# Kernel tuning notes

Hardware: AMD Instinct MI355X
Metric: run time of the kernel (lower is better)

The kernel has to match this reference:

```python
import jax, jax.numpy as jnp
import numpy as np

N, E, IN_DIM, HID = 100000, 1000000, 128, 64


def setup_inputs() -> dict:
    key = jax.random.key(0)
    ks = jax.random.split(key, 9)
    x = jax.random.normal(ks[0], (N, IN_DIM), dtype=jnp.float32)
    edge_index = jax.random.randint(ks[1], (2, E), 0, N, dtype=jnp.int32)
    edge_weight = jax.random.uniform(ks[2], (E,), dtype=jnp.float32)
    # GCNConv / Linear parameters (glorot-ish scaling)
    W1 = jax.random.normal(ks[3], (IN_DIM, HID), dtype=jnp.float32) / np.sqrt(IN_DIM)
    b1 = jnp.zeros((HID,), jnp.float32)
    W2 = jax.random.normal(ks[4], (HID, HID), dtype=jnp.float32) / np.sqrt(HID)
    b2 = jnp.zeros((HID,), jnp.float32)
    Wl = jax.random.normal(ks[5], (HID, 1), dtype=jnp.float32) / np.sqrt(HID)
    bl = jnp.zeros((1,), jnp.float32)
    return {"x": x, "edge_index": edge_index, "edge_weight": edge_weight,
            "W1": W1, "b1": b1, "W2": W2, "b2": b2, "Wl": Wl, "bl": bl}


def _propagate(h, src, dst, norm, num_nodes):
    # gather neighbor features, weight by norm, scatter-add to destinations
    msg = h[src] * norm[:, None]  # [E+N, HID]
    return jax.ops.segment_sum(msg, dst, num_segments=num_nodes)


def reference(x, edge_index, edge_weight, W1, b1, W2, b2, Wl, bl):
    n = x.shape[0]
    loop = jnp.arange(n, dtype=edge_index.dtype)
    # add self-loops with weight 1 (PyG GCNConv default)
    src = jnp.concatenate([edge_index[0], loop])
    dst = jnp.concatenate([edge_index[1], loop])
    ew = jnp.concatenate([edge_weight, jnp.ones((n,), x.dtype)])
    # symmetric normalization: D^-1/2 A D^-1/2
    deg = jax.ops.segment_sum(ew, dst, num_segments=n)
    dinv = jnp.where(deg > 0, jax.lax.rsqrt(deg), 0.0)
    norm = dinv[src] * ew * dinv[dst]  # [E+N]

    h = _propagate(x @ W1, src, dst, norm, n) + b1
    h = jax.nn.relu(h)  # dropout is identity in eval mode
    h = _propagate(h @ W2, src, dst, norm, n) + b2
    h = jax.nn.relu(h)
    return (h @ Wl + bl).squeeze(-1)  # [N]
```

## Files before the change

kernel.cpp:

```cpp
#include <hip/hip_runtime.h>

#define IN_DIM 128
#define HID    64
#define SCAN_B 256
#define RSIZE  16384
#define CSHIFT 14
#define CSIZE  (1 << CSHIFT)
#define NCMAX  64

typedef __attribute__((ext_vector_type(4))) _Float16 f16x4;
typedef __attribute__((ext_vector_type(8))) _Float16 f16x8;
typedef __attribute__((ext_vector_type(4))) float    f32x4;

__global__ void k_prep_w(const float* __restrict__ W1, const float* __restrict__ W2,
                         _Float16* __restrict__ W1T, _Float16* __restrict__ W2T) {
    int i = blockIdx.x * blockDim.x + threadIdx.x;
    if (i < IN_DIM * HID) { int k = i >> 6, c = i & 63; W1T[c * IN_DIM + k] = (_Float16)W1[i]; }
    if (i < HID * HID)    { int k = i >> 6, c = i & 63; W2T[c * HID + k]    = (_Float16)W2[i]; }
}

__global__ __launch_bounds__(256) void k_bin_hist(const int* __restrict__ dst,
                                                  unsigned short* __restrict__ hist16,
                                                  int* __restrict__ rank,
                                                  int n, int e) {
    __shared__ int cnt[RSIZE];
    int c = blockIdx.x, r = blockIdx.y;
    int tid = threadIdx.x;
    int4* c4 = (int4*)cnt;
    #pragma unroll
    for (int k = 0; k < RSIZE / 4 / 256; ++k) c4[tid + k * 256] = make_int4(0, 0, 0, 0);
    __syncthreads();

    int base = r * RSIZE;
    int i0 = c << CSHIFT;
    int i1 = min(e, i0 + CSIZE);
    for (int i = i0 + tid; i < i1; i += 256) {
        int d = dst[i];
        unsigned rel = (unsigned)(d - base);
        if (rel < RSIZE) rank[i] = atomicAdd(&cnt[rel], 1);
    }
    __syncthreads();

    size_t hb = (size_t)c * n;
    for (int j = tid; j < RSIZE; j += 256) {
        int v = base + j;
        if (v < n) hist16[hb + v] = (unsigned short)cnt[j];
    }
}

__global__ void k_chunk_scan(unsigned short* __restrict__ hist16,
                             int* __restrict__ offsets, int n, int nc) {
    int v = blockIdx.x * blockDim.x + threadIdx.x;
    if (v >= n) return;
    int run = 0;
    for (int c = 0; c < nc; ++c) {
        size_t idx = (size_t)c * n + v;
        int t = hist16[idx];
        hist16[idx] = (unsigned short)run;
        run += t;
    }
    offsets[v] = run;
}

__global__ __launch_bounds__(SCAN_B) void k_scan1(int* __restrict__ data,
                                                  int* __restrict__ blockSums, int n) {
    __shared__ int s[SCAN_B];
    int tid = threadIdx.x;
    int gid = blockIdx.x * SCAN_B + tid;
    int v = (gid < n) ? data[gid] : 0;
    s[tid] = v;
    __syncthreads();
    for (int off = 1; off < SCAN_B; off <<= 1) {
        int t = (tid >= off) ? s[tid - off] : 0;
        __syncthreads();
        s[tid] += t;
        __syncthreads();
    }
    if (gid < n) data[gid] = s[tid] - v;
    if (tid == SCAN_B - 1) blockSums[blockIdx.x] = s[tid];
}

__global__ __launch_bounds__(512) void k_scan2(int* __restrict__ blockSums, int nb) {
    __shared__ int s[512];
    int tid = threadIdx.x;
    int v = (tid < nb) ? blockSums[tid] : 0;
    s[tid] = v;
    __syncthreads();
    for (int off = 1; off < 512; off <<= 1) {
        int t = (tid >= off) ? s[tid - off] : 0;
        __syncthreads();
        s[tid] += t;
        __syncthreads();
    }
    if (tid < nb) blockSums[tid] = s[tid] - v;
}

__global__ __launch_bounds__(SCAN_B) void k_scan3(int* __restrict__ data,
                                                  const int* __restrict__ blockSums,
                                                  int n, int e) {
    int gid = blockIdx.x * SCAN_B + threadIdx.x;
    if (gid < n) {
        data[gid] += blockSums[blockIdx.x];
        if (gid == n - 1) data[n] = e;
    }
}

__global__ void k_scatter(const int* __restrict__ src, const int* __restrict__ dst,
                          const float* __restrict__ ew, const int* __restrict__ rank,
                          const int* __restrict__ offsets,
                          const unsigned short* __restrict__ hist16,
                          int2* __restrict__ sedge, int n, int e) {
    int i = blockIdx.x * blockDim.x + threadIdx.x;
    if (i >= e) return;
    int d = dst[i];
    int c = i >> CSHIFT;
    int pos = offsets[d] + (int)hist16[(size_t)c * n + d] + rank[i];
    sedge[pos] = make_int2(src[i], __float_as_int(ew[i]));
}

__global__ void k_deg_dinv(const int* __restrict__ rowOff, const int2* __restrict__ sedge,
                           float* __restrict__ dinv, int n) {
    int v = blockIdx.x * blockDim.x + threadIdx.x;
    if (v >= n) return;
    int s = rowOff[v], t = rowOff[v + 1];
    float a = 1.0f;
    for (int j = s; j < t; ++j) a += __int_as_float(sedge[j].y);
    dinv[v] = rsqrtf(a);
}


__global__ __launch_bounds__(256) void k_gemm1(const float* __restrict__ x,
                                               const _Float16* __restrict__ W1T,
                                               const float* __restrict__ dinv,
                                               _Float16* __restrict__ h0, int n) {
    __shared__ _Float16 sX[4][16 * IN_DIM];
    int tid  = threadIdx.x;
    int wave = tid >> 6, lane = tid & 63;
    int row0 = blockIdx.x * 64 + wave * 16;
    int col  = lane & 15, kg = lane >> 4;

    f16x8 bfrag[4][4];
    #pragma unroll
    for (int ks = 0; ks < 4; ++ks)
        #pragma unroll
        for (int ct = 0; ct < 4; ++ct)
            bfrag[ks][ct] = *(const f16x8*)(W1T + (ct * 16 + col) * IN_DIM + ks * 32 + kg * 8);

    _Float16* myX = sX[wave];
    #pragma unroll
    for (int it = 0; it < 8; ++it) {
        int idx = it * 64 + lane;
        int r = idx >> 5, c4 = idx & 31;
        int grow = row0 + r;
        float4 v = make_float4(0.f, 0.f, 0.f, 0.f);
        if (grow < n) v = ((const float4*)x)[(size_t)grow * 32 + c4];
        f16x4 h; h.x = (_Float16)v.x; h.y = (_Float16)v.y; h.z = (_Float16)v.z; h.w = (_Float16)v.w;
        int off = (r * 256 + c4 * 8) ^ ((r & 7) << 4);
        *(f16x4*)((char*)myX + off) = h;
    }
    __syncthreads();

    f32x4 acc[4];
    #pragma unroll
    for (int ct = 0; ct < 4; ++ct) acc[ct] = (f32x4){0.f, 0.f, 0.f, 0.f};

    int arow = lane & 15;
    #pragma unroll
    for (int ks = 0; ks < 4; ++ks) {
        int off = (arow * 256 + kg * 16 + ks * 64) ^ ((arow & 7) << 4);
        f16x8 af = *(const f16x8*)((const char*)myX + off);
        #pragma unroll
        for (int ct = 0; ct < 4; ++ct)
            acc[ct] = __builtin_amdgcn_mfma_f32_16x16x32_f16(af, bfrag[ks][ct], acc[ct], 0, 0, 0);
    }

    int crow0 = row0 + kg * 4;
    #pragma unroll
    for (int r = 0; r < 4; ++r) {
        int gr = crow0 + r;
        if (gr < n) {
            float dv = dinv[gr];
            #pragma unroll
            for (int ct = 0; ct < 4; ++ct)
                h0[(size_t)gr * HID + ct * 16 + col] = (_Float16)(acc[ct][r] * dv);
        }
    }
}


__global__ __launch_bounds__(256) void k_gemm2(const _Float16* __restrict__ h1,
                                               const _Float16* __restrict__ W2T,
                                               const float* __restrict__ dinv,
                                               _Float16* __restrict__ h2, int n) {
    __shared__ _Float16 sX[4][16 * HID];
    int tid  = threadIdx.x;
    int wave = tid >> 6, lane = tid & 63;
    int row0 = blockIdx.x * 64 + wave * 16;
    int col  = lane & 15, kg = lane >> 4;

    f16x8 bfrag[2][4];
    #pragma unroll
    for (int ks = 0; ks < 2; ++ks)
        #pragma unroll
        for (int ct = 0; ct < 4; ++ct)
            bfrag[ks][ct] = *(const f16x8*)(W2T + (ct * 16 + col) * HID + ks * 32 + kg * 8);

    _Float16* myX = sX[wave];
    #pragma unroll
    for (int it = 0; it < 4; ++it) {
        int idx = it * 64 + lane;
        int r = idx >> 4, c4 = idx & 15;
        int grow = row0 + r;
        f16x4 h = (f16x4){0, 0, 0, 0};
        if (grow < n) h = ((const f16x4*)h1)[(size_t)grow * 16 + c4];
        int off = (r * 128 + c4 * 8) ^ ((r & 7) << 4);
        *(f16x4*)((char*)myX + off) = h;
    }
    __syncthreads();

    f32x4 acc[4];
    #pragma unroll
    for (int ct = 0; ct < 4; ++ct) acc[ct] = (f32x4){0.f, 0.f, 0.f, 0.f};

    int arow = lane & 15;
    #pragma unroll
    for (int ks = 0; ks < 2; ++ks) {
        int off = (arow * 128 + kg * 16 + ks * 64) ^ ((arow & 7) << 4);
        f16x8 af = *(const f16x8*)((const char*)myX + off);
        #pragma unroll
        for (int ct = 0; ct < 4; ++ct)
            acc[ct] = __builtin_amdgcn_mfma_f32_16x16x32_f16(af, bfrag[ks][ct], acc[ct], 0, 0, 0);
    }

    int crow0 = row0 + kg * 4;
    #pragma unroll
    for (int r = 0; r < 4; ++r) {
        int gr = crow0 + r;
        if (gr < n) {
            float dv = dinv[gr];
            #pragma unroll
            for (int ct = 0; ct < 4; ++ct)
                h2[(size_t)gr * HID + ct * 16 + col] = (_Float16)(acc[ct][r] * dv);
        }
    }
}


__global__ __launch_bounds__(256) void k_prop1(const int* __restrict__ rowOff,
                                               const int2* __restrict__ sedge,
                                               const _Float16* __restrict__ hin,
                                               const float* __restrict__ dinv,
                                               const float* __restrict__ b1,
                                               _Float16* __restrict__ hout, int n) {
    int wave = (blockIdx.x * blockDim.x + threadIdx.x) >> 6;
    int lane = threadIdx.x & 63;
    int g    = lane >> 3;
    int gl   = lane & 7;
    int node = wave * 8 + g;
    bool valid = node < n;
    int nd = valid ? node : 0;

    int start = rowOff[nd];
    int end   = valid ? rowOff[nd + 1] : start;
    float di  = dinv[nd];
    float4 bbA = ((const float4*)b1)[gl * 2];
    float4 bbB = ((const float4*)b1)[gl * 2 + 1];

    f16x8 sv = *(const f16x8*)(hin + (size_t)nd * HID + gl * 8);
    float a[8];
    #pragma unroll
    for (int t = 0; t < 8; ++t) a[t] = (float)sv[t];

    int j = start;
    for (; j + 4 <= end; j += 4) {
        int2 e0 = sedge[j], e1 = sedge[j + 1], e2 = sedge[j + 2], e3 = sedge[j + 3];
        f16x8 v0 = *(const f16x8*)(hin + (size_t)e0.x * HID + gl * 8);
        f16x8 v1 = *(const f16x8*)(hin + (size_t)e1.x * HID + gl * 8);
        f16x8 v2 = *(const f16x8*)(hin + (size_t)e2.x * HID + gl * 8);
        f16x8 v3 = *(const f16x8*)(hin + (size_t)e3.x * HID + gl * 8);
        float w0 = __int_as_float(e0.y), w1 = __int_as_float(e1.y);
        float w2 = __int_as_float(e2.y), w3 = __int_as_float(e3.y);
        #pragma unroll
        for (int t = 0; t < 8; ++t) a[t] = fmaf((float)v0[t], w0, a[t]);
        #pragma unroll
        for (int t = 0; t < 8; ++t) a[t] = fmaf((float)v1[t], w1, a[t]);
        #pragma unroll
        for (int t = 0; t < 8; ++t) a[t] = fmaf((float)v2[t], w2, a[t]);
        #pragma unroll
        for (int t = 0; t < 8; ++t) a[t] = fmaf((float)v3[t], w3, a[t]);
    }
    if (j < end) {
        #pragma unroll
        for (int k = 0; k < 4; ++k) {
            int idx = j + k;
            int cl  = idx < end ? idx : j;
            int2 ed = sedge[cl];
            float w = idx < end ? __int_as_float(ed.y) : 0.0f;
            f16x8 v = *(const f16x8*)(hin + (size_t)ed.x * HID + gl * 8);
            #pragma unroll
            for (int t = 0; t < 8; ++t) a[t] = fmaf((float)v[t], w, a[t]);
        }
    }

    if (valid) {
        f16x8 o;
        o[0] = (_Float16)fmaxf(fmaf(a[0], di, bbA.x), 0.0f);
        o[1] = (_Float16)fmaxf(fmaf(a[1], di, bbA.y), 0.0f);
        o[2] = (_Float16)fmaxf(fmaf(a[2], di, bbA.z), 0.0f);
        o[3] = (_Float16)fmaxf(fmaf(a[3], di, bbA.w), 0.0f);
        o[4] = (_Float16)fmaxf(fmaf(a[4], di, bbB.x), 0.0f);
        o[5] = (_Float16)fmaxf(fmaf(a[5], di, bbB.y), 0.0f);
        o[6] = (_Float16)fmaxf(fmaf(a[6], di, bbB.z), 0.0f);
        o[7] = (_Float16)fmaxf(fmaf(a[7], di, bbB.w), 0.0f);
        *(f16x8*)(hout + (size_t)node * HID + gl * 8) = o;
    }
}

__global__ __launch_bounds__(256) void k_prop2_final(const int* __restrict__ rowOff,
                                                     const int2* __restrict__ sedge,
                                                     const _Float16* __restrict__ hin,
                                                     const float* __restrict__ dinv,
                                                     const float* __restrict__ b2,
                                                     const float* __restrict__ Wl,
                                                     const float* __restrict__ bl,
                                                     float* __restrict__ out, int n) {
    int wave = (blockIdx.x * blockDim.x + threadIdx.x) >> 6;
    int lane = threadIdx.x & 63;
    int g    = lane >> 3;
    int gl   = lane & 7;
    int node = wave * 8 + g;
    bool valid = node < n;
    int nd = valid ? node : 0;

    int start = rowOff[nd];
    int end   = valid ? rowOff[nd + 1] : start;
    float di  = dinv[nd];
    float4 bbA = ((const float4*)b2)[gl * 2];
    float4 bbB = ((const float4*)b2)[gl * 2 + 1];
    float4 wlA = ((const float4*)Wl)[gl * 2];
    float4 wlB = ((const float4*)Wl)[gl * 2 + 1];

    f16x8 sv = *(const f16x8*)(hin + (size_t)nd * HID + gl * 8);
    float a[8];
    #pragma unroll
    for (int t = 0; t < 8; ++t) a[t] = (float)sv[t];

    int j = start;
    for (; j + 4 <= end; j += 4) {
        int2 e0 = sedge[j], e1 = sedge[j + 1], e2 = sedge[j + 2], e3 = sedge[j + 3];
        f16x8 v0 = *(const f16x8*)(hin + (size_t)e0.x * HID + gl * 8);
        f16x8 v1 = *(const f16x8*)(hin + (size_t)e1.x * HID + gl * 8);
        f16x8 v2 = *(const f16x8*)(hin + (size_t)e2.x * HID + gl * 8);
        f16x8 v3 = *(const f16x8*)(hin + (size_t)e3.x * HID + gl * 8);
        float w0 = __int_as_float(e0.y), w1 = __int_as_float(e1.y);
        float w2 = __int_as_float(e2.y), w3 = __int_as_float(e3.y);
        #pragma unroll
        for (int t = 0; t < 8; ++t) a[t] = fmaf((float)v0[t], w0, a[t]);
        #pragma unroll
        for (int t = 0; t < 8; ++t) a[t] = fmaf((float)v1[t], w1, a[t]);
        #pragma unroll
        for (int t = 0; t < 8; ++t) a[t] = fmaf((float)v2[t], w2, a[t]);
        #pragma unroll
        for (int t = 0; t < 8; ++t) a[t] = fmaf((float)v3[t], w3, a[t]);
    }
    if (j < end) {
        #pragma unroll
        for (int k = 0; k < 4; ++k) {
            int idx = j + k;
            int cl  = idx < end ? idx : j;
            int2 ed = sedge[cl];
            float w = idx < end ? __int_as_float(ed.y) : 0.0f;
            f16x8 v = *(const f16x8*)(hin + (size_t)ed.x * HID + gl * 8);
            #pragma unroll
            for (int t = 0; t < 8; ++t) a[t] = fmaf((float)v[t], w, a[t]);
        }
    }

    float bb[8] = {bbA.x, bbA.y, bbA.z, bbA.w, bbB.x, bbB.y, bbB.z, bbB.w};
    float wl[8] = {wlA.x, wlA.y, wlA.z, wlA.w, wlB.x, wlB.y, wlB.z, wlB.w};
    float v = 0.0f;
    #pragma unroll
    for (int t = 0; t < 8; ++t)
        v += fmaxf(fmaf(a[t], di, bb[t]), 0.0f) * wl[t];
    #pragma unroll
    for (int off = 1; off < 8; off <<= 1)
        v += __shfl_xor(v, off);
    if (valid && gl == 0) out[node] = v + bl[0];
}


static inline char* align16(char* p) {
    return (char*)(((uintptr_t)p + 15) & ~(uintptr_t)15);
}

extern "C" void kernel_launch(void* const* d_in, const int* in_sizes, int n_in,
                              void* d_out, int out_size, void* d_ws, size_t ws_size,
                              hipStream_t stream) {
    const float* x   = (const float*)d_in[0];
    const int*   ei  = (const int*)d_in[1];
    const float* ew  = (const float*)d_in[2];
    const float* W1  = (const float*)d_in[3];
    const float* b1  = (const float*)d_in[4];
    const float* W2  = (const float*)d_in[5];
    const float* b2  = (const float*)d_in[6];
    const float* Wl  = (const float*)d_in[7];
    const float* bl  = (const float*)d_in[8];

    const int n = in_sizes[0] / IN_DIM;
    const int e = in_sizes[2];
    const int* src = ei;
    const int* dst = ei + e;

    float* out = (float*)d_out;
    const int B256 = 256;
    const int nScanBlocks = (n + SCAN_B - 1) / SCAN_B;
    const int nc = (e + CSIZE - 1) >> CSHIFT;
    const int nr = (n + RSIZE - 1) / RSIZE;

    char* p = (char*)d_ws;
    int2*           sedge   = (int2*)p;            p += (size_t)e * 8;
    float*          dinv    = (float*)p;           p += (size_t)n * 4;
    int*            offsets = (int*)p;             p += ((size_t)n + 1) * 4;
    p = align16(p);
    int*            bsums   = (int*)p;             p += 512 * 4;
    int*            rank    = (int*)p;             p += (size_t)e * 4;
    p = align16(p);
    unsigned short* hist16  = (unsigned short*)p;  p += (size_t)NCMAX * n * 2;
    _Float16*       W1T     = (_Float16*)p;        p += IN_DIM * HID * 2;
    _Float16*       W2T     = (_Float16*)p;        p += HID * HID * 2;
    p = align16(p);
    _Float16*       A       = (_Float16*)p;        p += (size_t)n * HID * 2;
    _Float16*       B       = (_Float16*)p;        p += (size_t)n * HID * 2;

    k_prep_w<<<(IN_DIM * HID + B256 - 1) / B256, B256, 0, stream>>>(W1, W2, W1T, W2T);

    dim3 binGrid(nc, nr);
    k_bin_hist<<<binGrid, B256, 0, stream>>>(dst, hist16, rank, n, e);

    k_chunk_scan<<<(n + B256 - 1) / B256, B256, 0, stream>>>(hist16, offsets, n, nc);

    k_scan1<<<nScanBlocks, SCAN_B, 0, stream>>>(offsets, bsums, n);
    k_scan2<<<1, 512, 0, stream>>>(bsums, nScanBlocks);
    k_scan3<<<nScanBlocks, SCAN_B, 0, stream>>>(offsets, bsums, n, e);

    k_scatter<<<(e + B256 - 1) / B256, B256, 0, stream>>>(src, dst, ew, rank,
                                                         offsets, hist16, sedge, n, e);

    k_deg_dinv<<<(n + B256 - 1) / B256, B256, 0, stream>>>(offsets, sedge, dinv, n);

    const int gemmBlocks = (n + 63) / 64;
    const int propBlocks = (n + 31) / 32;

    k_gemm1<<<gemmBlocks, B256, 0, stream>>>(x, W1T, dinv, A, n);
    k_prop1<<<propBlocks, B256, 0, stream>>>(offsets, sedge, A, dinv, b1, B, n);

    k_gemm2<<<gemmBlocks, B256, 0, stream>>>(B, W2T, dinv, A, n);
    k_prop2_final<<<propBlocks, B256, 0, stream>>>(offsets, sedge, A, dinv,
                                                   b2, Wl, bl, out, n);
}
```

Measured before the change: 199.9 us.

## Fuse CSR build into cooperative kernel and unroll edge gather by eight

Merges weight prep, destination binning, chunk scan, the block-level scan, scatter and degree computation into one cooperative kernel separated by grid-wide syncs. This removes several dependent launches and the final scan pass by folding block sums into the offset lookups. The propagation kernels now gather eight neighbor rows per iteration instead of four, to keep more loads in flight. The cost is grid-sync overhead, fewer threads in the scatter phase, and extra register pressure in the propagation loops. A multi-kernel fallback is kept for when cooperative residency is not possible.

```diff
diff --git a/kernel.cpp b/kernel.cpp
--- a/kernel.cpp
+++ b/kernel.cpp
@@ -1,4 +1,7 @@
 #include <hip/hip_runtime.h>
+#include <hip/hip_cooperative_groups.h>
+
+namespace cg = cooperative_groups;
 
 #define IN_DIM 128
 #define HID    64
@@ -11,6 +14,119 @@
 typedef __attribute__((ext_vector_type(4))) _Float16 f16x4;
 typedef __attribute__((ext_vector_type(8))) _Float16 f16x8;
 typedef __attribute__((ext_vector_type(4))) float    f32x4;
+
+__global__ __launch_bounds__(256, 2) void k_build(
+    const float* __restrict__ W1, const float* __restrict__ W2,
+    _Float16* __restrict__ W1T, _Float16* __restrict__ W2T,
+    const int* __restrict__ src, const int* __restrict__ dst,
+    const float* __restrict__ ew,
+    unsigned short* __restrict__ hist16, int* __restrict__ rank,
+    int* __restrict__ offsets, int* __restrict__ bsums,
+    int2* __restrict__ sedge, float* __restrict__ dinv,
+    int n, int e, int nc, int nr, int nTiles)
+{
+    __shared__ int cnt[RSIZE];
+    cg::grid_group grid = cg::this_grid();
+    const int nb  = nc * nr;
+    const int b   = blockIdx.x;
+    const int tid = threadIdx.x;
+
+    if (b < nb) {
+        int c = b % nc, r = b / nc;
+        int4* c4 = (int4*)cnt;
+        #pragma unroll
+        for (int k = tid; k < RSIZE / 4; k += 256) c4[k] = make_int4(0, 0, 0, 0);
+        __syncthreads();
+        int base = r * RSIZE;
+        int i0 = c << CSHIFT;
+        int i1 = min(e, i0 + CSIZE);
+        for (int i = i0 + tid; i < i1; i += 256) {
+            int d = dst[i];
+            unsigned rel = (unsigned)(d - base);
+            if (rel < RSIZE) rank[i] = atomicAdd(&cnt[rel], 1);
+        }
+        __syncthreads();
+        size_t hb = (size_t)c * n;
+        for (int j = tid; j < RSIZE; j += 256) {
+            int v = base + j;
+            if (v < n) hist16[hb + v] = (unsigned short)cnt[j];
+        }
+    } else {
+        int t = (b - nb) * 256 + tid;
+        for (int i = t; i < IN_DIM * HID; i += 512) {
+            int k = i >> 6, c2 = i & 63;
+            W1T[c2 * IN_DIM + k] = (_Float16)W1[i];
+        }
+        for (int i = t; i < HID * HID; i += 512) {
+            int k = i >> 6, c2 = i & 63;
+            W2T[c2 * HID + k] = (_Float16)W2[i];
+        }
+    }
+    grid.sync();
+
+    int gt = b * 256 + tid;
+    int total = 0;
+    if (gt < n) {
+        int run = 0;
+        for (int c = 0; c < nc; ++c) {
+            size_t idx = (size_t)c * n + gt;
+            int t0 = hist16[idx];
+            hist16[idx] = (unsigned short)run;
+            run += t0;
+        }
+        total = run;
+    }
+    __syncthreads();
+    cnt[tid] = total;
+    __syncthreads();
+    for (int off = 1; off < 256; off <<= 1) {
+        int t2 = (tid >= off) ? cnt[tid - off] : 0;
+        __syncthreads();
+        cnt[tid] += t2;
+        __syncthreads();
+    }
+    if (gt < n) offsets[gt] = cnt[tid] - total;
+    if (tid == 255 && b < nTiles) bsums[b] = cnt[255];
+    grid.sync();
+
+    if (b == 0) {
+        int v0 = (2 * tid     < nTiles) ? bsums[2 * tid]     : 0;
+        int v1 = (2 * tid + 1 < nTiles) ? bsums[2 * tid + 1] : 0;
+        __syncthreads();
+        cnt[tid] = v0 + v1;
+        __syncthreads();
+        for (int off = 1; off < 256; off <<= 1) {
+            int t2 = (tid >= off) ? cnt[tid - off] : 0;
+            __syncthreads();
+            cnt[tid] += t2;
+            __syncthreads();
+        }
+        int pexcl = cnt[tid] - (v0 + v1);
+        if (2 * tid     < nTiles) bsums[2 * tid]     = pexcl;
+        if (2 * tid + 1 < nTiles) bsums[2 * tid + 1] = pexcl + v0;
+    }
+    grid.sync();
+
+    {
+        int stride = gridDim.x * 256;
+        for (int i = gt; i < e; i += stride) {
+            int d = dst[i];
+            int c = i >> CSHIFT;
+            int pos = offsets[d] + bsums[d >> 8] + (int)hist16[(size_t)c * n + d] + rank[i];
+            sedge[pos] = make_int2(src[i], __float_as_int(ew[i]));
+        }
+    }
+    grid.sync();
+
+    if (gt < n) {
+        int s0 = offsets[gt] + bsums[gt >> 8];
+        int s1 = (gt == n - 1) ? e : (offsets[gt + 1] + bsums[(gt + 1) >> 8]);
+        float a = 1.0f;
+        for (int j = s0; j < s1; ++j) a += __int_as_float(sedge[j].y);
+        dinv[gt] = rsqrtf(a);
+    }
+}
+
 
 __global__ void k_prep_w(const float* __restrict__ W1, const float* __restrict__ W2,
                          _Float16* __restrict__ W1T, _Float16* __restrict__ W2T) {
@@ -28,9 +144,8 @@
     int tid = threadIdx.x;
     int4* c4 = (int4*)cnt;
     #pragma unroll
-    for (int k = 0; k < RSIZE / 4 / 256; ++k) c4[tid + k * 256] = make_int4(0, 0, 0, 0);
-    __syncthreads();
-
+    for (int k = tid; k < RSIZE / 4; k += 256) c4[k] = make_int4(0, 0, 0, 0);
+    __syncthreads();
     int base = r * RSIZE;
     int i0 = c << CSHIFT;
     int i1 = min(e, i0 + CSIZE);
@@ -40,7 +155,6 @@
         if (rel < RSIZE) rank[i] = atomicAdd(&cnt[rel], 1);
     }
     __syncthreads();
-
     size_t hb = (size_t)c * n;
     for (int j = tid; j < RSIZE; j += 256) {
         int v = base + j;
@@ -95,36 +209,28 @@
     if (tid < nb) blockSums[tid] = s[tid] - v;
 }
 
-__global__ __launch_bounds__(SCAN_B) void k_scan3(int* __restrict__ data,
-                                                  const int* __restrict__ blockSums,
-                                                  int n, int e) {
-    int gid = blockIdx.x * SCAN_B + threadIdx.x;
-    if (gid < n) {
-        data[gid] += blockSums[blockIdx.x];
-        if (gid == n - 1) data[n] = e;
-    }
-}
-
-__global__ void k_scatter(const int* __restrict__ src, const int* __restrict__ dst,
-                          const float* __restrict__ ew, const int* __restrict__ rank,
-                          const int* __restrict__ offsets,
-                          const unsigned short* __restrict__ hist16,
-                          int2* __restrict__ sedge, int n, int e) {
+__global__ void k_scatter_fb(const int* __restrict__ src, const int* __restrict__ dst,
+                             const float* __restrict__ ew, const int* __restrict__ rank,
+                             const int* __restrict__ offsets, const int* __restrict__ bsums,
+                             const unsigned short* __restrict__ hist16,
+                             int2* __restrict__ sedge, int n, int e) {
     int i = blockIdx.x * blockDim.x + threadIdx.x;
     if (i >= e) return;
     int d = dst[i];
     int c = i >> CSHIFT;
-    int pos = offsets[d] + (int)hist16[(size_t)c * n + d] + rank[i];
+    int pos = offsets[d] + bsums[d >> 8] + (int)hist16[(size_t)c * n + d] + rank[i];
     sedge[pos] = make_int2(src[i], __float_as_int(ew[i]));
 }
 
-__global__ void k_deg_dinv(const int* __restrict__ rowOff, const int2* __restrict__ sedge,
-                           float* __restrict__ dinv, int n) {
+__global__ void k_deg_dinv_fb(const int* __restrict__ offsets, const int* __restrict__ bsums,
+                              const int2* __restrict__ sedge, float* __restrict__ dinv,
+                              int n, int e) {
     int v = blockIdx.x * blockDim.x + threadIdx.x;
     if (v >= n) return;
-    int s = rowOff[v], t = rowOff[v + 1];
+    int s0 = offsets[v] + bsums[v >> 8];
+    int s1 = (v == n - 1) ? e : (offsets[v + 1] + bsums[(v + 1) >> 8]);
     float a = 1.0f;
-    for (int j = s; j < t; ++j) a += __int_as_float(sedge[j].y);
+    for (int j = s0; j < s1; ++j) a += __int_as_float(sedge[j].y);
     dinv[v] = rsqrtf(a);
 }
 
@@ -187,7 +293,6 @@
     }
 }
 
-
 __global__ __launch_bounds__(256) void k_gemm2(const _Float16* __restrict__ h1,
                                                const _Float16* __restrict__ W2T,
                                                const float* __restrict__ dinv,
@@ -246,12 +351,13 @@
 }
 
 
-__global__ __launch_bounds__(256) void k_prop1(const int* __restrict__ rowOff,
+__global__ __launch_bounds__(256) void k_prop1(const int* __restrict__ offR,
+                                               const int* __restrict__ bsums,
                                                const int2* __restrict__ sedge,
                                                const _Float16* __restrict__ hin,
                                                const float* __restrict__ dinv,
                                                const float* __restrict__ b1,
-                                               _Float16* __restrict__ hout, int n) {
+                                               _Float16* __restrict__ hout, int n, int e) {
     int wave = (blockIdx.x * blockDim.x + threadIdx.x) >> 6;
     int lane = threadIdx.x & 63;
     int g    = lane >> 3;
@@ -260,9 +366,13 @@
     bool valid = node < n;
     int nd = valid ? node : 0;
 
-    int start = rowOff[nd];
-    int end   = valid ? rowOff[nd + 1] : start;
-    float di  = dinv[nd];
+    int start = offR[nd] + bsums[nd >> 8];
+    int end;
+    if (!valid)            end = start;
+    else if (nd == n - 1)  end = e;
+    else                   end = offR[nd + 1] + bsums[(nd + 1) >> 8];
+
+    float di = dinv[nd];
     float4 bbA = ((const float4*)b1)[gl * 2];
     float4 bbB = ((const float4*)b1)[gl * 2 + 1];
 
@@ -272,26 +382,22 @@
     for (int t = 0; t < 8; ++t) a[t] = (float)sv[t];
 
     int j = start;
-    for (; j + 4 <= end; j += 4) {
-        int2 e0 = sedge[j], e1 = sedge[j + 1], e2 = sedge[j + 2], e3 = sedge[j + 3];
-        f16x8 v0 = *(const f16x8*)(hin + (size_t)e0.x * HID + gl * 8);
-        f16x8 v1 = *(const f16x8*)(hin + (size_t)e1.x * HID + gl * 8);
-        f16x8 v2 = *(const f16x8*)(hin + (size_t)e2.x * HID + gl * 8);
-        f16x8 v3 = *(const f16x8*)(hin + (size_t)e3.x * HID + gl * 8);
-        float w0 = __int_as_float(e0.y), w1 = __int_as_float(e1.y);
-        float w2 = __int_as_float(e2.y), w3 = __int_as_float(e3.y);
-        #pragma unroll
-        for (int t = 0; t < 8; ++t) a[t] = fmaf((float)v0[t], w0, a[t]);
-        #pragma unroll
-        for (int t = 0; t < 8; ++t) a[t] = fmaf((float)v1[t], w1, a[t]);
-        #pragma unroll
-        for (int t = 0; t < 8; ++t) a[t] = fmaf((float)v2[t], w2, a[t]);
-        #pragma unroll
-        for (int t = 0; t < 8; ++t) a[t] = fmaf((float)v3[t], w3, a[t]);
+    for (; j + 8 <= end; j += 8) {
+        int2 ed[8]; f16x8 v[8]; float w[8];
+        #pragma unroll
+        for (int k = 0; k < 8; ++k) ed[k] = sedge[j + k];
+        #pragma unroll
+        for (int k = 0; k < 8; ++k) v[k] = *(const f16x8*)(hin + (size_t)ed[k].x * HID + gl * 8);
+        #pragma unroll
+        for (int k = 0; k < 8; ++k) w[k] = __int_as_float(ed[k].y);
+        #pragma unroll
+        for (int k = 0; k < 8; ++k)
+            #pragma unroll
+            for (int t = 0; t < 8; ++t) a[t] = fmaf((float)v[k][t], w[k], a[t]);
     }
     if (j < end) {
         #pragma unroll
-        for (int k = 0; k < 4; ++k) {
+        for (int k = 0; k < 8; ++k) {
             int idx = j + k;
             int cl  = idx < end ? idx : j;
             int2 ed = sedge[cl];
@@ -316,14 +422,15 @@
     }
 }
 
-__global__ __launch_bounds__(256) void k_prop2_final(const int* __restrict__ rowOff,
+__global__ __launch_bounds__(256) void k_prop2_final(const int* __restrict__ offR,
+                                                     const int* __restrict__ bsums,
                                                      const int2* __restrict__ sedge,
                                                      const _Float16* __restrict__ hin,
                                                      const float* __restrict__ dinv,
                                                      const float* __restrict__ b2,
                                                      const float* __restrict__ Wl,
                                                      const float* __restrict__ bl,
-                                                     float* __restrict__ out, int n) {
+                                                     float* __restrict__ out, int n, int e) {
     int wave = (blockIdx.x * blockDim.x + threadIdx.x) >> 6;
     int lane = threadIdx.x & 63;
     int g    = lane >> 3;
@@ -332,9 +439,13 @@
     bool valid = node < n;
     int nd = valid ? node : 0;
 
-    int start = rowOff[nd];
-    int end   = valid ? rowOff[nd + 1] : start;
-    float di  = dinv[nd];
+    int start = offR[nd] + bsums[nd >> 8];
+    int end;
+    if (!valid)            end = start;
+    else if (nd == n - 1)  end = e;
+    else                   end = offR[nd + 1] + bsums[(nd + 1) >> 8];
+
+    float di = dinv[nd];
     float4 bbA = ((const float4*)b2)[gl * 2];
     float4 bbB = ((const float4*)b2)[gl * 2 + 1];
     float4 wlA = ((const float4*)Wl)[gl * 2];
@@ -346,26 +457,22 @@
     for (int t = 0; t < 8; ++t) a[t] = (float)sv[t];
 
     int j = start;
-    for (; j + 4 <= end; j += 4) {
-        int2 e0 = sedge[j], e1 = sedge[j + 1], e2 = sedge[j + 2], e3 = sedge[j + 3];
-        f16x8 v0 = *(const f16x8*)(hin + (size_t)e0.x * HID + gl * 8);
-        f16x8 v1 = *(const f16x8*)(hin + (size_t)e1.x * HID + gl * 8);
-        f16x8 v2 = *(const f16x8*)(hin + (size_t)e2.x * HID + gl * 8);
-        f16x8 v3 = *(const f16x8*)(hin + (size_t)e3.x * HID + gl * 8);
-        float w0 = __int_as_float(e0.y), w1 = __int_as_float(e1.y);
-        float w2 = __int_as_float(e2.y), w3 = __int_as_float(e3.y);
-        #pragma unroll
-        for (int t = 0; t < 8; ++t) a[t] = fmaf((float)v0[t], w0, a[t]);
-        #pragma unroll
-        for (int t = 0; t < 8; ++t) a[t] = fmaf((float)v1[t], w1, a[t]);
-        #pragma unroll
-        for (int t = 0; t < 8; ++t) a[t] = fmaf((float)v2[t], w2, a[t]);
-        #pragma unroll
-        for (int t = 0; t < 8; ++t) a[t] = fmaf((float)v3[t], w3, a[t]);
+    for (; j + 8 <= end; j += 8) {
+        int2 ed[8]; f16x8 v[8]; float w[8];
+        #pragma unroll
+        for (int k = 0; k < 8; ++k) ed[k] = sedge[j + k];
+        #pragma unroll
+        for (int k = 0; k < 8; ++k) v[k] = *(const f16x8*)(hin + (size_t)ed[k].x * HID + gl * 8);
+        #pragma unroll
+        for (int k = 0; k < 8; ++k) w[k] = __int_as_float(ed[k].y);
+        #pragma unroll
+        for (int k = 0; k < 8; ++k)
+            #pragma unroll
+            for (int t = 0; t < 8; ++t) a[t] = fmaf((float)v[k][t], w[k], a[t]);
     }
     if (j < end) {
         #pragma unroll
-        for (int k = 0; k < 4; ++k) {
+        for (int k = 0; k < 8; ++k) {
             int idx = j + k;
             int cl  = idx < end ? idx : j;
             int2 ed = sedge[cl];
@@ -413,9 +520,10 @@
 
     float* out = (float*)d_out;
     const int B256 = 256;
-    const int nScanBlocks = (n + SCAN_B - 1) / SCAN_B;
     const int nc = (e + CSIZE - 1) >> CSHIFT;
     const int nr = (n + RSIZE - 1) / RSIZE;
+    const int nTiles = (n + 255) / 256;
+    const int buildBlocks = nc * nr + 2;
 
     char* p = (char*)d_ws;
     int2*           sedge   = (int2*)p;            p += (size_t)e * 8;
@@ -432,29 +540,43 @@
     _Float16*       A       = (_Float16*)p;        p += (size_t)n * HID * 2;
     _Float16*       B       = (_Float16*)p;        p += (size_t)n * HID * 2;
 
-    k_prep_w<<<(IN_DIM * HID + B256 - 1) / B256, B256, 0, stream>>>(W1, W2, W1T, W2T);
-
-    dim3 binGrid(nc, nr);
-    k_bin_hist<<<binGrid, B256, 0, stream>>>(dst, hist16, rank, n, e);
-
-    k_chunk_scan<<<(n + B256 - 1) / B256, B256, 0, stream>>>(hist16, offsets, n, nc);
-
-    k_scan1<<<nScanBlocks, SCAN_B, 0, stream>>>(offsets, bsums, n);
-    k_scan2<<<1, 512, 0, stream>>>(bsums, nScanBlocks);
-    k_scan3<<<nScanBlocks, SCAN_B, 0, stream>>>(offsets, bsums, n, e);
-
-    k_scatter<<<(e + B256 - 1) / B256, B256, 0, stream>>>(src, dst, ew, rank,
-                                                         offsets, hist16, sedge, n, e);
-
-    k_deg_dinv<<<(n + B256 - 1) / B256, B256, 0, stream>>>(offsets, sedge, dinv, n);
+    int dev = 0;
+    hipGetDevice(&dev);
+    int nCU = 0;
+    hipDeviceGetAttribute(&nCU, hipDeviceAttributeMultiprocessorCount, dev);
+    int maxB = 0;
+    hipOccupancyMaxActiveBlocksPerMultiprocessor(&maxB, k_build, 256, 0);
+    bool coop = (nCU > 0 && maxB * nCU >= buildBlocks) && nTiles <= 512;
+
+    if (coop) {
+        int n_ = n, e_ = e, nc_ = nc, nr_ = nr, nT_ = nTiles;
+        void* args[] = {(void*)&W1, (void*)&W2, (void*)&W1T, (void*)&W2T,
+                        (void*)&src, (void*)&dst, (void*)&ew,
+                        (void*)&hist16, (void*)&rank, (void*)&offsets, (void*)&bsums,
+                        (void*)&sedge, (void*)&dinv,
+                        (void*)&n_, (void*)&e_, (void*)&nc_, (void*)&nr_, (void*)&nT_};
+        hipLaunchCooperativeKernel(k_build, dim3(buildBlocks), dim3(256), args, 0, stream);
+    } else {
+        k_prep_w<<<(IN_DIM * HID + B256 - 1) / B256, B256, 0, stream>>>(W1, W2, W1T, W2T);
+        dim3 binGrid(nc, nr);
+        k_bin_hist<<<binGrid, B256, 0, stream>>>(dst, hist16, rank, n, e);
+        k_chunk_scan<<<(n + B256 - 1) / B256, B256, 0, stream>>>(hist16, offsets, n, nc);
+        k_scan1<<<nTiles, SCAN_B, 0, stream>>>(offsets, bsums, n);
+        k_scan2<<<1, 512, 0, stream>>>(bsums, nTiles);
+        k_scatter_fb<<<(e + B256 - 1) / B256, B256, 0, stream>>>(src, dst, ew, rank,
+                                                                offsets, bsums, hist16,
+                                                                sedge, n, e);
+        k_deg_dinv_fb<<<(n + B256 - 1) / B256, B256, 0, stream>>>(offsets, bsums,
+                                                                 sedge, dinv, n, e);
+    }
 
     const int gemmBlocks = (n + 63) / 64;
     const int propBlocks = (n + 31) / 32;
 
     k_gemm1<<<gemmBlocks, B256, 0, stream>>>(x, W1T, dinv, A, n);
-    k_prop1<<<propBlocks, B256, 0, stream>>>(offsets, sedge, A, dinv, b1, B, n);
+    k_prop1<<<propBlocks, B256, 0, stream>>>(offsets, bsums, sedge, A, dinv, b1, B, n, e);
 
     k_gemm2<<<gemmBlocks, B256, 0, stream>>>(B, W2T, dinv, A, n);
-    k_prop2_final<<<propBlocks, B256, 0, stream>>>(offsets, sedge, A, dinv,
-                                                   b2, Wl, bl, out, n);
-}
+    k_prop2_final<<<propBlocks, B256, 0, stream>>>(offsets, bsums, sedge, A, dinv,
+                                                   b2, Wl, bl, out, n, e);
+}
```

Result: slower. 434.8 us (+117.4%).

## Replace CSR build with two-level bucket sort and unroll propagation gather by 8

Applied to the files above, without the earlier changes.

Replaces the per-node histogram, multi-kernel scan and scatter CSR construction with a two-level bucket sort. Edges are first counted and scattered into coarse buckets of 256 destination nodes, then a per-bucket kernel does a fine local sort and also computes degrees and dinv. Weight transposition is folded into the count kernel, which cuts the launch count and the large hist16/rank traffic. The propagation loops now issue 8 gathers per iteration instead of 4 to raise memory-level parallelism, at the cost of more registers and nondeterministic edge order inside a node.

```diff
diff --git a/kernel.cpp b/kernel.cpp
--- a/kernel.cpp
+++ b/kernel.cpp
@@ -2,130 +2,137 @@
 
 #define IN_DIM 128
 #define HID    64
-#define SCAN_B 256
-#define RSIZE  16384
-#define CSHIFT 14
-#define CSIZE  (1 << CSHIFT)
-#define NCMAX  64
+#define NCHUNK 128
+#define BWSH   8
+#define BW     (1 << BWSH)
 
 typedef __attribute__((ext_vector_type(4))) _Float16 f16x4;
 typedef __attribute__((ext_vector_type(8))) _Float16 f16x8;
 typedef __attribute__((ext_vector_type(4))) float    f32x4;
 
-__global__ void k_prep_w(const float* __restrict__ W1, const float* __restrict__ W2,
-                         _Float16* __restrict__ W1T, _Float16* __restrict__ W2T) {
-    int i = blockIdx.x * blockDim.x + threadIdx.x;
-    if (i < IN_DIM * HID) { int k = i >> 6, c = i & 63; W1T[c * IN_DIM + k] = (_Float16)W1[i]; }
-    if (i < HID * HID)    { int k = i >> 6, c = i & 63; W2T[c * HID + k]    = (_Float16)W2[i]; }
-}
-
-__global__ __launch_bounds__(256) void k_bin_hist(const int* __restrict__ dst,
-                                                  unsigned short* __restrict__ hist16,
-                                                  int* __restrict__ rank,
-                                                  int n, int e) {
-    __shared__ int cnt[RSIZE];
-    int c = blockIdx.x, r = blockIdx.y;
-    int tid = threadIdx.x;
-    int4* c4 = (int4*)cnt;
-    #pragma unroll
-    for (int k = 0; k < RSIZE / 4 / 256; ++k) c4[tid + k * 256] = make_int4(0, 0, 0, 0);
-    __syncthreads();
-
-    int base = r * RSIZE;
-    int i0 = c << CSHIFT;
-    int i1 = min(e, i0 + CSIZE);
+__global__ __launch_bounds__(256) void k_bcount(const int* __restrict__ dst,
+                                                int* __restrict__ counts,
+                                                const float* __restrict__ W1,
+                                                const float* __restrict__ W2,
+                                                _Float16* __restrict__ W1T,
+                                                _Float16* __restrict__ W2T,
+                                                int e, int nbk, int ech) {
+    int c = blockIdx.x, tid = threadIdx.x;
+    if (c >= NCHUNK) {
+        int t = (c - NCHUNK) * 256 + tid;
+        for (int i = t; i < IN_DIM * HID; i += 512) {
+            int k = i >> 6, cc = i & 63;
+            W1T[cc * IN_DIM + k] = (_Float16)W1[i];
+        }
+        for (int i = t; i < HID * HID; i += 512) {
+            int k = i >> 6, cc = i & 63;
+            W2T[cc * HID + k] = (_Float16)W2[i];
+        }
+        return;
+    }
+    __shared__ int cnt[512];
+    cnt[tid] = 0; cnt[tid + 256] = 0;
+    __syncthreads();
+    int i0 = c * ech, i1 = min(e, i0 + ech);
+    for (int i = i0 + tid; i < i1; i += 256)
+        atomicAdd(&cnt[dst[i] >> BWSH], 1);
+    __syncthreads();
+    for (int b = tid; b < nbk; b += 256) counts[c * nbk + b] = cnt[b];
+}
+
+__global__ __launch_bounds__(512) void k_bscan(int* __restrict__ counts,
+                                               int* __restrict__ bstart,
+                                               int* __restrict__ offsets,
+                                               int n, int e, int nbk) {
+    __shared__ int s[512];
+    int b = threadIdx.x;
+    int run = 0;
+    if (b < nbk) {
+        for (int c = 0; c < NCHUNK; ++c) {
+            int t = counts[c * nbk + b];
+            counts[c * nbk + b] = run;
+            run += t;
+        }
+    }
+    s[b] = run;
+    __syncthreads();
+    for (int off = 1; off < 512; off <<= 1) {
+        int t = (b >= off) ? s[b - off] : 0;
+        __syncthreads();
+        s[b] += t;
+        __syncthreads();
+    }
+    int excl = s[b] - run;
+    if (b < nbk) {
+        bstart[b] = excl;
+        for (int c = 0; c < NCHUNK; ++c) counts[c * nbk + b] += excl;
+    }
+    if (b == 0) { bstart[nbk] = e; offsets[n] = e; }
+}
+
+__global__ __launch_bounds__(256) void k_bscatter(const int* __restrict__ src,
+                                                  const int* __restrict__ dst,
+                                                  const float* __restrict__ ew,
+                                                  const int* __restrict__ starts,
+                                                  int2* __restrict__ tmpe,
+                                                  unsigned short* __restrict__ tmpl,
+                                                  int e, int nbk, int ech) {
+    __shared__ int cur[512];
+    int c = blockIdx.x, tid = threadIdx.x;
+    for (int b = tid; b < nbk; b += 256) cur[b] = starts[c * nbk + b];
+    __syncthreads();
+    int i0 = c * ech, i1 = min(e, i0 + ech);
     for (int i = i0 + tid; i < i1; i += 256) {
         int d = dst[i];
-        unsigned rel = (unsigned)(d - base);
-        if (rel < RSIZE) rank[i] = atomicAdd(&cnt[rel], 1);
-    }
-    __syncthreads();
-
-    size_t hb = (size_t)c * n;
-    for (int j = tid; j < RSIZE; j += 256) {
-        int v = base + j;
-        if (v < n) hist16[hb + v] = (unsigned short)cnt[j];
-    }
-}
-
-__global__ void k_chunk_scan(unsigned short* __restrict__ hist16,
-                             int* __restrict__ offsets, int n, int nc) {
-    int v = blockIdx.x * blockDim.x + threadIdx.x;
-    if (v >= n) return;
-    int run = 0;
-    for (int c = 0; c < nc; ++c) {
-        size_t idx = (size_t)c * n + v;
-        int t = hist16[idx];
-        hist16[idx] = (unsigned short)run;
-        run += t;
-    }
-    offsets[v] = run;
-}
-
-__global__ __launch_bounds__(SCAN_B) void k_scan1(int* __restrict__ data,
-                                                  int* __restrict__ blockSums, int n) {
-    __shared__ int s[SCAN_B];
-    int tid = threadIdx.x;
-    int gid = blockIdx.x * SCAN_B + tid;
-    int v = (gid < n) ? data[gid] : 0;
-    s[tid] = v;
-    __syncthreads();
-    for (int off = 1; off < SCAN_B; off <<= 1) {
-        int t = (tid >= off) ? s[tid - off] : 0;
+        int b = d >> BWSH;
+        int pos = atomicAdd(&cur[b], 1);
+        tmpe[pos] = make_int2(src[i], __float_as_int(ew[i]));
+        tmpl[pos] = (unsigned short)(d & (BW - 1));
+    }
+}
+
+__global__ __launch_bounds__(256) void k_bfine(const int* __restrict__ bstart,
+                                               const int2* __restrict__ tmpe,
+                                               const unsigned short* __restrict__ tmpl,
+                                               int2* __restrict__ sedge,
+                                               int* __restrict__ offsets,
+                                               float* __restrict__ dinv, int n) {
+    __shared__ int   cnt[256];
+    __shared__ float wsum[256];
+    __shared__ int   lsc[256];
+    __shared__ int   cur[256];
+    int b = blockIdx.x, tid = threadIdx.x;
+    int bs = bstart[b], be = bstart[b + 1];
+    cnt[tid] = 0; wsum[tid] = 0.0f;
+    __syncthreads();
+    for (int j = bs + tid; j < be; j += 256) {
+        int ld = tmpl[j];
+        atomicAdd(&cnt[ld], 1);
+        atomicAdd(&wsum[ld], __int_as_float(tmpe[j].y));
+    }
+    __syncthreads();
+    int v = cnt[tid];
+    lsc[tid] = v;
+    __syncthreads();
+    for (int off = 1; off < 256; off <<= 1) {
+        int t = (tid >= off) ? lsc[tid - off] : 0;
         __syncthreads();
-        s[tid] += t;
+        lsc[tid] += t;
         __syncthreads();
     }
-    if (gid < n) data[gid] = s[tid] - v;
-    if (tid == SCAN_B - 1) blockSums[blockIdx.x] = s[tid];
-}
-
-__global__ __launch_bounds__(512) void k_scan2(int* __restrict__ blockSums, int nb) {
-    __shared__ int s[512];
-    int tid = threadIdx.x;
-    int v = (tid < nb) ? blockSums[tid] : 0;
-    s[tid] = v;
-    __syncthreads();
-    for (int off = 1; off < 512; off <<= 1) {
-        int t = (tid >= off) ? s[tid - off] : 0;
-        __syncthreads();
-        s[tid] += t;
-        __syncthreads();
-    }
-    if (tid < nb) blockSums[tid] = s[tid] - v;
-}
-
-__global__ __launch_bounds__(SCAN_B) void k_scan3(int* __restrict__ data,
-                                                  const int* __restrict__ blockSums,
-                                                  int n, int e) {
-    int gid = blockIdx.x * SCAN_B + threadIdx.x;
-    if (gid < n) {
-        data[gid] += blockSums[blockIdx.x];
-        if (gid == n - 1) data[n] = e;
-    }
-}
-
-__global__ void k_scatter(const int* __restrict__ src, const int* __restrict__ dst,
-                          const float* __restrict__ ew, const int* __restrict__ rank,
-                          const int* __restrict__ offsets,
-                          const unsigned short* __restrict__ hist16,
-                          int2* __restrict__ sedge, int n, int e) {
-    int i = blockIdx.x * blockDim.x + threadIdx.x;
-    if (i >= e) return;
-    int d = dst[i];
-    int c = i >> CSHIFT;
-    int pos = offsets[d] + (int)hist16[(size_t)c * n + d] + rank[i];
-    sedge[pos] = make_int2(src[i], __float_as_int(ew[i]));
-}
-
-__global__ void k_deg_dinv(const int* __restrict__ rowOff, const int2* __restrict__ sedge,
-                           float* __restrict__ dinv, int n) {
-    int v = blockIdx.x * blockDim.x + threadIdx.x;
-    if (v >= n) return;
-    int s = rowOff[v], t = rowOff[v + 1];
-    float a = 1.0f;
-    for (int j = s; j < t; ++j) a += __int_as_float(sedge[j].y);
-    dinv[v] = rsqrtf(a);
+    int excl = lsc[tid] - v;
+    int node = b * BW + tid;
+    if (node < n) {
+        offsets[node] = bs + excl;
+        dinv[node] = rsqrtf(1.0f + wsum[tid]);
+    }
+    cur[tid] = excl;
+    __syncthreads();
+    for (int j = bs + tid; j < be; j += 256) {
+        int ld = tmpl[j];
+        int pos = bs + atomicAdd(&cur[ld], 1);
+        sedge[pos] = tmpe[j];
+    }
 }
 
 
@@ -187,7 +194,6 @@
     }
 }
 
-
 __global__ __launch_bounds__(256) void k_gemm2(const _Float16* __restrict__ h1,
                                                const _Float16* __restrict__ W2T,
                                                const float* __restrict__ dinv,
@@ -246,7 +252,7 @@
 }
 
 
-__global__ __launch_bounds__(256) void k_prop1(const int* __restrict__ rowOff,
+__global__ __launch_bounds__(256) void k_prop1(const int* __restrict__ offR,
                                                const int2* __restrict__ sedge,
                                                const _Float16* __restrict__ hin,
                                                const float* __restrict__ dinv,
@@ -260,9 +266,10 @@
     bool valid = node < n;
     int nd = valid ? node : 0;
 
-    int start = rowOff[nd];
-    int end   = valid ? rowOff[nd + 1] : start;
-    float di  = dinv[nd];
+    int start = offR[nd];
+    int end   = valid ? offR[nd + 1] : start;
+
+    float di = dinv[nd];
     float4 bbA = ((const float4*)b1)[gl * 2];
     float4 bbB = ((const float4*)b1)[gl * 2 + 1];
 
@@ -272,26 +279,22 @@
     for (int t = 0; t < 8; ++t) a[t] = (float)sv[t];
 
     int j = start;
-    for (; j + 4 <= end; j += 4) {
-        int2 e0 = sedge[j], e1 = sedge[j + 1], e2 = sedge[j + 2], e3 = sedge[j + 3];
-        f16x8 v0 = *(const f16x8*)(hin + (size_t)e0.x * HID + gl * 8);
-        f16x8 v1 = *(const f16x8*)(hin + (size_t)e1.x * HID + gl * 8);
-        f16x8 v2 = *(const f16x8*)(hin + (size_t)e2.x * HID + gl * 8);
-        f16x8 v3 = *(const f16x8*)(hin + (size_t)e3.x * HID + gl * 8);
-        float w0 = __int_as_float(e0.y), w1 = __int_as_float(e1.y);
-        float w2 = __int_as_float(e2.y), w3 = __int_as_float(e3.y);
-        #pragma unroll
-        for (int t = 0; t < 8; ++t) a[t] = fmaf((float)v0[t], w0, a[t]);
-        #pragma unroll
-        for (int t = 0; t < 8; ++t) a[t] = fmaf((float)v1[t], w1, a[t]);
-        #pragma unroll
-        for (int t = 0; t < 8; ++t) a[t] = fmaf((float)v2[t], w2, a[t]);
-        #pragma unroll
-        for (int t = 0; t < 8; ++t) a[t] = fmaf((float)v3[t], w3, a[t]);
+    for (; j + 8 <= end; j += 8) {
+        int2 ed[8]; f16x8 v[8]; float w[8];
+        #pragma unroll
+        for (int k = 0; k < 8; ++k) ed[k] = sedge[j + k];
+        #pragma unroll
+        for (int k = 0; k < 8; ++k) v[k] = *(const f16x8*)(hin + (size_t)ed[k].x * HID + gl * 8);
+        #pragma unroll
+        for (int k = 0; k < 8; ++k) w[k] = __int_as_float(ed[k].y);
+        #pragma unroll
+        for (int k = 0; k < 8; ++k)
+            #pragma unroll
+            for (int t = 0; t < 8; ++t) a[t] = fmaf((float)v[k][t], w[k], a[t]);
     }
     if (j < end) {
         #pragma unroll
-        for (int k = 0; k < 4; ++k) {
+        for (int k = 0; k < 8; ++k) {
             int idx = j + k;
             int cl  = idx < end ? idx : j;
             int2 ed = sedge[cl];
@@ -316,7 +319,7 @@
     }
 }
 
-__global__ __launch_bounds__(256) void k_prop2_final(const int* __restrict__ rowOff,
+__global__ __launch_bounds__(256) void k_prop2_final(const int* __restrict__ offR,
                                                      const int2* __restrict__ sedge,
                                                      const _Float16* __restrict__ hin,
                                                      const float* __restrict__ dinv,
@@ -332,9 +335,10 @@
     bool valid = node < n;
     int nd = valid ? node : 0;
 
-    int start = rowOff[nd];
-    int end   = valid ? rowOff[nd + 1] : start;
-    float di  = dinv[nd];
+    int start = offR[nd];
+    int end   = valid ? offR[nd + 1] : start;
+
+    float di = dinv[nd];
     float4 bbA = ((const float4*)b2)[gl * 2];
     float4 bbB = ((const float4*)b2)[gl * 2 + 1];
     float4 wlA = ((const float4*)Wl)[gl * 2];
@@ -346,26 +350,22 @@
     for (int t = 0; t < 8; ++t) a[t] = (float)sv[t];
 
     int j = start;
-    for (; j + 4 <= end; j += 4) {
-        int2 e0 = sedge[j], e1 = sedge[j + 1], e2 = sedge[j + 2], e3 = sedge[j + 3];
-        f16x8 v0 = *(const f16x8*)(hin + (size_t)e0.x * HID + gl * 8);
-        f16x8 v1 = *(const f16x8*)(hin + (size_t)e1.x * HID + gl * 8);
-        f16x8 v2 = *(const f16x8*)(hin + (size_t)e2.x * HID + gl * 8);
-        f16x8 v3 = *(const f16x8*)(hin + (size_t)e3.x * HID + gl * 8);
-        float w0 = __int_as_float(e0.y), w1 = __int_as_float(e1.y);
-        float w2 = __int_as_float(e2.y), w3 = __int_as_float(e3.y);
-        #pragma unroll
-        for (int t = 0; t < 8; ++t) a[t] = fmaf((float)v0[t], w0, a[t]);
-        #pragma unroll
-        for (int t = 0; t < 8; ++t) a[t] = fmaf((float)v1[t], w1, a[t]);
-        #pragma unroll
-        for (int t = 0; t < 8; ++t) a[t] = fmaf((float)v2[t], w2, a[t]);
-        #pragma unroll
-        for (int t = 0; t < 8; ++t) a[t] = fmaf((float)v3[t], w3, a[t]);
+    for (; j + 8 <= end; j += 8) {
+        int2 ed[8]; f16x8 v[8]; float w[8];
+        #pragma unroll
+        for (int k = 0; k < 8; ++k) ed[k] = sedge[j + k];
+        #pragma unroll
+        for (int k = 0; k < 8; ++k) v[k] = *(const f16x8*)(hin + (size_t)ed[k].x * HID + gl * 8);
+        #pragma unroll
+        for (int k = 0; k < 8; ++k) w[k] = __int_as_float(ed[k].y);
+        #pragma unroll
+        for (int k = 0; k < 8; ++k)
+            #pragma unroll
+            for (int t = 0; t < 8; ++t) a[t] = fmaf((float)v[k][t], w[k], a[t]);
     }
     if (j < end) {
         #pragma unroll
-        for (int k = 0; k < 4; ++k) {
+        for (int k = 0; k < 8; ++k) {
             int idx = j + k;
             int cl  = idx < end ? idx : j;
             int2 ed = sedge[cl];
@@ -413,40 +413,30 @@
 
     float* out = (float*)d_out;
     const int B256 = 256;
-    const int nScanBlocks = (n + SCAN_B - 1) / SCAN_B;
-    const int nc = (e + CSIZE - 1) >> CSHIFT;
-    const int nr = (n + RSIZE - 1) / RSIZE;
+    const int nbk = (n + BW - 1) >> BWSH;
+    const int ech = (e + NCHUNK - 1) / NCHUNK;
 
     char* p = (char*)d_ws;
     int2*           sedge   = (int2*)p;            p += (size_t)e * 8;
+    int2*           tmpe    = (int2*)p;            p += (size_t)e * 8;
+    unsigned short* tmpl    = (unsigned short*)p;  p += (size_t)e * 2;
+    p = align16(p);
     float*          dinv    = (float*)p;           p += (size_t)n * 4;
     int*            offsets = (int*)p;             p += ((size_t)n + 1) * 4;
     p = align16(p);
-    int*            bsums   = (int*)p;             p += 512 * 4;
-    int*            rank    = (int*)p;             p += (size_t)e * 4;
+    int*            counts  = (int*)p;             p += (size_t)NCHUNK * nbk * 4;
+    int*            bstart  = (int*)p;             p += ((size_t)nbk + 1) * 4;
     p = align16(p);
-    unsigned short* hist16  = (unsigned short*)p;  p += (size_t)NCMAX * n * 2;
     _Float16*       W1T     = (_Float16*)p;        p += IN_DIM * HID * 2;
     _Float16*       W2T     = (_Float16*)p;        p += HID * HID * 2;
     p = align16(p);
     _Float16*       A       = (_Float16*)p;        p += (size_t)n * HID * 2;
     _Float16*       B       = (_Float16*)p;        p += (size_t)n * HID * 2;
 
-    k_prep_w<<<(IN_DIM * HID + B256 - 1) / B256, B256, 0, stream>>>(W1, W2, W1T, W2T);
-
-    dim3 binGrid(nc, nr);
-    k_bin_hist<<<binGrid, B256, 0, stream>>>(dst, hist16, rank, n, e);
-
-    k_chunk_scan<<<(n + B256 - 1) / B256, B256, 0, stream>>>(hist16, offsets, n, nc);
-
-    k_scan1<<<nScanBlocks, SCAN_B, 0, stream>>>(offsets, bsums, n);
-    k_scan2<<<1, 512, 0, stream>>>(bsums, nScanBlocks);
-    k_scan3<<<nScanBlocks, SCAN_B, 0, stream>>>(offsets, bsums, n, e);
-
-    k_scatter<<<(e + B256 - 1) / B256, B256, 0, stream>>>(src, dst, ew, rank,
-                                                         offsets, hist16, sedge, n, e);
-
-    k_deg_dinv<<<(n + B256 - 1) / B256, B256, 0, stream>>>(offsets, sedge, dinv, n);
+    k_bcount  <<<NCHUNK + 2, B256, 0, stream>>>(dst, counts, W1, W2, W1T, W2T, e, nbk, ech);
+    k_bscan   <<<1, 512, 0, stream>>>(counts, bstart, offsets, n, e, nbk);
+    k_bscatter<<<NCHUNK, B256, 0, stream>>>(src, dst, ew, counts, tmpe, tmpl, e, nbk, ech);
+    k_bfine   <<<nbk, B256, 0, stream>>>(bstart, tmpe, tmpl, sedge, offsets, dinv, n);
 
     const int gemmBlocks = (n + 63) / 64;
     const int propBlocks = (n + 31) / 32;
```

After: 199.1 us. No clear change (-0.4%).
